# Kernel tuning notes

Measured on AMD Instinct MI355X. Metric: run time of the kernel, lower is better.

Reference implementation:

```python
import jax, jax.numpy as jnp
import numpy as np

B, T, W, L, H, TW = 4, 8192, 1024, 1024, 8, 4
D = L // H
A_SCALE = 8.0  # RG-LRU 'c' constant


def setup_inputs() -> dict:
    key = jax.random.key(0)
    ks = jax.random.split(key, 12)
    nrm = lambda k, shape, std: jax.random.normal(k, shape, jnp.float32) * std
    x = jax.random.normal(ks[0], (B, T, W), jnp.float32)
    segment_pos = jnp.tile(jnp.arange(T, dtype=jnp.int32)[None, :], (B, 1))
    Wy = nrm(ks[1], (W, L), (1.0 / W) ** 0.5)
    by = jnp.zeros((L,), jnp.float32)
    Wx = nrm(ks[2], (W, L), (1.0 / W) ** 0.5)
    bx = jnp.zeros((L,), jnp.float32)
    Wout = nrm(ks[3], (L, W), (1.0 / L) ** 0.5)
    bout = jnp.zeros((W,), jnp.float32)
    conv_w = nrm(ks[4], (TW, L), (1.0 / (TW * L)) ** 0.5)
    conv_b = jnp.zeros((L,), jnp.float32)
    # a_param init: radius in [0.9, 0.999], stored pre-softplus (Griffin rnn_param_init)
    u = jax.random.uniform(ks[5], (L,), jnp.float32)
    a_real = 0.5 * jnp.log(u * (0.999 ** 2 - 0.9 ** 2) + 0.9 ** 2 + 1e-8)  # negative
    a_param = jnp.log(jnp.expm1(-a_real))  # softplus(a_param) == -a_real
    igate_w = nrm(ks[6], (H, D, D), (1.0 / D) ** 0.5)
    igate_b = jnp.zeros((H, D), jnp.float32)
    agate_w = nrm(ks[7], (H, D, D), (1.0 / D) ** 0.5)
    agate_b = jnp.zeros((H, D), jnp.float32)
    return dict(x=x, segment_pos=segment_pos, Wy=Wy, by=by, Wx=Wx, bx=bx,
                conv_w=conv_w, conv_b=conv_b, a_param=a_param,
                igate_w=igate_w, igate_b=igate_b, agate_w=agate_w, agate_b=agate_b,
                Wout=Wout, bout=bout)


def _forward(x, segment_pos, Wy, by, Wx, bx, conv_w, conv_b, a_param,
             igate_w, igate_b, agate_w, agate_b, Wout, bout):
    pos = segment_pos  # [B, T]
    # gating branch
    y = jax.nn.gelu(x @ Wy + by, approximate=True)  # [B,T,L]
    # recurrent branch: linear_x -> causal depthwise conv1d -> RG-LRU
    u = x @ Wx + bx  # [B,T,L]
    acc = jnp.zeros_like(u)
    for i in range(TW):  # small fixed temporal width
        shift = TW - 1 - i
        u_sh = jnp.pad(u, ((0, 0), (shift, 0), (0, 0)))[:, :T]
        valid = (pos >= shift)[..., None]  # zero across segment boundaries
        acc = acc + jnp.where(valid, u_sh * conv_w[i], 0.0)
    u = acc + conv_b  # [B,T,L]
    # RG-LRU gates (block-diagonal per head)
    ur = u.reshape(B, T, H, D)
    gate_x = jax.nn.sigmoid(jnp.einsum('bthd,hde->bthe', ur, igate_w) + igate_b).reshape(B, T, L)
    gate_a = jax.nn.sigmoid(jnp.einsum('bthd,hde->bthe', ur, agate_w) + agate_b).reshape(B, T, L)
    log_a = -A_SCALE * gate_a * jax.nn.softplus(a_param)  # [B,T,L]
    a = jnp.exp(log_a)
    multiplier = jnp.sqrt(1.0 - jnp.exp(2.0 * log_a))
    reset = (pos == 0)[..., None]
    normed_x = (u * gate_x) * jnp.where(reset, 1.0, multiplier)
    a_m = jnp.where(reset, 0.0, a)
    # linear recurrence h_t = a_t * h_{t-1} + normed_x_t via associative scan
    def combine(c1, c2):
        a1, b1 = c1
        a2, b2 = c2
        return (a1 * a2, a2 * b1 + b2)
    _, h = jax.lax.associative_scan(combine, (a_m, normed_x), axis=1)
    return (h * y) @ Wout + bout  # [B,T,W]


def reference(x, segment_pos, Wy, by, Wx, bx, conv_w, conv_b, a_param,
              igate_w, igate_b, agate_w, agate_b, Wout, bout):
    return _forward(x, segment_pos, Wy, by, Wx, bx, conv_w, conv_b, a_param,
                    igate_w, igate_b, agate_w, agate_b, Wout, bout)
```

## Files before the change

kernel.cpp:

```cpp
#include <hip/hip_runtime.h>
#include <cstdint>
#include <cstddef>

#define B_ 4
#define T_ 8192
#define W_ 1024
#define L_ 1024
#define H_ 8
#define D_ 128
#define TW_ 4
#define BT_ (B_*T_)
#define CHUNK_ 32
#define NCH_ (T_/CHUNK_)

typedef __bf16 bf16_t;
typedef __bf16 bf16x8 __attribute__((ext_vector_type(8)));
typedef float  f32x4  __attribute__((ext_vector_type(4)));

__device__ __forceinline__ float  bf2f(bf16_t x){ return (float)x; }
__device__ __forceinline__ bf16_t f2bf(float x){ return (bf16_t)x; }

__device__ __forceinline__ float rcp_ (float x){ return __builtin_amdgcn_rcpf(x); }
__device__ __forceinline__ float sqrt_(float x){ return __builtin_amdgcn_sqrtf(x); }
__device__ __forceinline__ float exp2_(float x){ return __builtin_amdgcn_exp2f(x); }
__device__ __forceinline__ float log2_(float x){ return __builtin_amdgcn_logf(x); }
#define LOG2E_ 1.4426950408889634f

__device__ __forceinline__ float sigmoid_fast(float z){
  return rcp_(1.0f + exp2_(-LOG2E_*z));
}
__device__ __forceinline__ float softplus_fast(float x){
  return (x > 15.0f) ? x : 0.6931471805599453f * log2_(1.0f + exp2_(LOG2E_*x));
}
__device__ __forceinline__ float gelu_fast(float z){
  float g = 0.7978845608028654f*(z + 0.044715f*z*z*z);
  float e = exp2_(-2.8853900817779268f*fabsf(g));
  float th = (1.0f - e)*rcp_(1.0f + e);
  th = copysignf(th, g);
  return 0.5f*z*(1.0f + th);
}

__device__ __forceinline__ void stage16(const bf16_t* g, bf16_t* l){
  __builtin_amdgcn_global_load_lds((const __attribute__((address_space(1))) void*)g,
                                   (__attribute__((address_space(3))) void*)l, 16, 0, 0);
}
__device__ __forceinline__ void stage_tile(const bf16_t* __restrict__ gbase, int ldg,
                                           bf16_t* lds, int wave, int lane){
  #pragma unroll
  for (int c2 = 0; c2 < 2; ++c2){
    int chunk = wave*2 + c2;
    int row = chunk*16 + (lane >> 2);
    int col = (lane & 3)*8;
    stage16(gbase + (size_t)row*ldg + col, lds + chunk*512 + lane*8);
  }
}

__global__ void __launch_bounds__(256) cvt_kernel(const float* __restrict__ in,
                                                  bf16_t* __restrict__ out, int n8){
  int g = blockIdx.x*256 + threadIdx.x;
  if (g >= n8) return;
  f32x4 a = *(const f32x4*)(in + (size_t)g*8);
  f32x4 b = *(const f32x4*)(in + (size_t)g*8 + 4);
  bf16x8 o;
  #pragma unroll
  for (int e=0;e<4;e++){ o[e] = f2bf(a[e]); o[4+e] = f2bf(b[e]); }
  *(bf16x8*)(out + (size_t)g*8) = o;
}

__global__ void __launch_bounds__(256) transpose_f2b(const float* __restrict__ in,
                                                     bf16_t* __restrict__ out, int R, int C){
  __shared__ float tile[32][33];
  size_t mb = (size_t)blockIdx.z * R * C;
  int c0 = blockIdx.x*32, r0 = blockIdx.y*32;
  int tx = threadIdx.x, ty = threadIdx.y;
  #pragma unroll
  for (int i = ty; i < 32; i += 8)
    tile[i][tx] = in[mb + (size_t)(r0+i)*C + c0 + tx];
  __syncthreads();
  #pragma unroll
  for (int i = ty; i < 32; i += 8)
    out[mb + (size_t)(c0+i)*R + r0 + tx] = f2bf(tile[tx][i]);
}

__global__ void __launch_bounds__(256,2) gemm_xw_kernel(
    const bf16_t* __restrict__ X,
    const bf16_t* __restrict__ WyT, const bf16_t* __restrict__ WxT,
    const float* __restrict__ by,  const float* __restrict__ bx,
    bf16_t* __restrict__ Y, bf16_t* __restrict__ U0)
{
  __shared__ __align__(16) bf16_t As [128*32];
  __shared__ __align__(16) bf16_t Bys[128*32];
  __shared__ __align__(16) bf16_t Bxs[128*32];
  __shared__ __align__(16) bf16_t scr_g[4][1280];
  const int K = W_;
  int tid = threadIdx.x, wave = tid>>6, lane = tid&63;
  int wm = wave>>1, wn = wave&1, q = lane>>4, ml = lane&15;
  int lin = blockIdx.x;
  int nl = (lin & 7)*256 + (lin >> 3);
  int bm = nl >> 3, j = nl & 7;
  const bf16_t* Wyp = WyT + (size_t)j*128*K;
  const bf16_t* Wxp = WxT + (size_t)j*128*K;
  f32x4 accY[4][4] = {}, accX[4][4] = {};
  for (int k0 = 0; k0 < K; k0 += 32){
    stage_tile(X + (size_t)bm*128*K + k0, K, As, wave, lane);
    stage_tile(Wyp + k0, K, Bys, wave, lane);
    stage_tile(Wxp + k0, K, Bxs, wave, lane);
    __syncthreads();
    bf16x8 af[4], bvy[4], bvx[4];
    #pragma unroll
    for (int i=0;i<4;i++) af[i]  = *(const bf16x8*)(As  + (wm*64 + i*16 + ml)*32 + q*8);
    #pragma unroll
    for (int i=0;i<4;i++) bvy[i] = *(const bf16x8*)(Bys + (wn*64 + i*16 + ml)*32 + q*8);
    #pragma unroll
    for (int i=0;i<4;i++) bvx[i] = *(const bf16x8*)(Bxs + (wn*64 + i*16 + ml)*32 + q*8);
    #pragma unroll
    for (int i=0;i<4;i++)
      #pragma unroll
      for (int n=0;n<4;n++){
        accY[i][n] = __builtin_amdgcn_mfma_f32_16x16x32_bf16(af[i], bvy[n], accY[i][n], 0,0,0);
        accX[i][n] = __builtin_amdgcn_mfma_f32_16x16x32_bf16(af[i], bvx[n], accX[i][n], 0,0,0);
      }
    __syncthreads();
  }
  float bbY[4], bbX[4];
  #pragma unroll
  for (int n=0;n<4;n++){
    int col = j*128 + wn*64 + n*16 + ml;
    bbY[n] = by[col]; bbX[n] = bx[col];
  }
  bf16_t* s0 = scr_g[wave];
  bf16_t* s1 = s0 + 640;
  int rrow = lane>>2, cgp = lane&3;
  size_t mbase = (size_t)bm*128 + wm*64;
  #pragma unroll
  for (int i=0;i<4;i++){
    size_t grow = mbase + i*16 + rrow;
    int gc = j*128 + wn*64 + cgp*8;
    #pragma unroll
    for (int n=0;n<4;n++){
      bf16_t* sp = (n<2) ? s0 : s1;
      #pragma unroll
      for (int r=0;r<4;r++)
        sp[(q*4+r)*40 + (n&1)*16 + ml] = f2bf(gelu_fast(accY[i][n][r] + bbY[n]));
    }
    {
      bf16x8 v0 = *(const bf16x8*)(s0 + rrow*40 + cgp*8);
      bf16x8 v1 = *(const bf16x8*)(s1 + rrow*40 + cgp*8);
      *(bf16x8*)(Y + grow*L_ + gc)      = v0;
      *(bf16x8*)(Y + grow*L_ + gc + 32) = v1;
    }
    #pragma unroll
    for (int n=0;n<4;n++){
      bf16_t* sp = (n<2) ? s0 : s1;
      #pragma unroll
      for (int r=0;r<4;r++)
        sp[(q*4+r)*40 + (n&1)*16 + ml] = f2bf(accX[i][n][r] + bbX[n]);
    }
    {
      bf16x8 v0 = *(const bf16x8*)(s0 + rrow*40 + cgp*8);
      bf16x8 v1 = *(const bf16x8*)(s1 + rrow*40 + cgp*8);
      *(bf16x8*)(U0 + grow*L_ + gc)      = v0;
      *(bf16x8*)(U0 + grow*L_ + gc + 32) = v1;
    }
  }
}

__global__ void __launch_bounds__(256,2) gate_kernel(
    const bf16_t* __restrict__ U0,
    const bf16_t* __restrict__ igTw, const bf16_t* __restrict__ agTw,
    const float* __restrict__ igb,  const float* __restrict__ agb,
    const float* __restrict__ a_param,
    const float* __restrict__ conv_w, const float* __restrict__ conv_b,
    const int* __restrict__ segpos,
    bf16_t* __restrict__ XN, bf16_t* __restrict__ L2A)
{
  __shared__ __align__(16) bf16_t As[4*128*32];
  __shared__ __align__(16) bf16_t scr_g[4][2560];
  int tid = threadIdx.x, wave = tid>>6, lane = tid&63;
  int wm = wave>>1, wn = wave&1, q = lane>>4, ml = lane&15;
  int bm = blockIdx.x, h = blockIdx.y;

  {
    int cg = tid & 15, rg = tid >> 4;
    int col = cg*8;
    int kcc = col >> 5, c32 = col & 31;
    const bf16_t* up = U0 + ((size_t)bm*128 + (size_t)rg*8)*L_ + h*128 + col;
    f32x4 wta[4], wtb[4];
    #pragma unroll
    for (int s=0;s<4;s++){
      wta[s] = *(const f32x4*)(conv_w + (size_t)(3-s)*L_ + h*128 + col);
      wtb[s] = *(const f32x4*)(conv_w + (size_t)(3-s)*L_ + h*128 + col + 4);
    }
    f32x4 cba = *(const f32x4*)(conv_b + h*128 + col);
    f32x4 cbb = *(const f32x4*)(conv_b + h*128 + col + 4);
    bool first = (bm & 63) == 0;
    int r0 = rg*8;
    bf16x8 zero8 = {};
    bf16x8 m1 = (!first || r0 >= 1) ? *(const bf16x8*)(up - 1*L_) : zero8;
    bf16x8 m2 = (!first || r0 >= 2) ? *(const bf16x8*)(up - 2*L_) : zero8;
    bf16x8 m3 = (!first || r0 >= 3) ? *(const bf16x8*)(up - 3*L_) : zero8;
    #pragma unroll
    for (int r=0;r<8;r++){
      bf16x8 cur = *(const bf16x8*)(up + (size_t)r*L_);
      bf16x8 ov;
      #pragma unroll
      for (int e=0;e<4;e++){
        float v0 = cba[e] + bf2f(cur[e])*wta[0][e] + bf2f(m1[e])*wta[1][e]
                          + bf2f(m2[e])*wta[2][e] + bf2f(m3[e])*wta[3][e];
        float v1 = cbb[e] + bf2f(cur[4+e])*wtb[0][e] + bf2f(m1[4+e])*wtb[1][e]
                          + bf2f(m2[4+e])*wtb[2][e] + bf2f(m3[4+e])*wtb[3][e];
        ov[e] = f2bf(v0); ov[4+e] = f2bf(v1);
      }
      *(bf16x8*)(As + kcc*4096 + (size_t)(r0+r)*32 + c32) = ov;
      m3 = m2; m2 = m1; m1 = cur;
    }
  }
  __syncthreads();

  const bf16_t* igp = igTw + (size_t)h*D_*D_;
  const bf16_t* agp = agTw + (size_t)h*D_*D_;
  f32x4 ax[4][4] = {}, aa[4][4] = {};
  #pragma unroll
  for (int kc=0; kc<4; ++kc){
    bf16x8 af[4], bx_[4], ba_[4];
    #pragma unroll
    for (int i=0;i<4;i++) af[i]  = *(const bf16x8*)(As + kc*4096 + (wm*64 + i*16 + ml)*32 + q*8);
    #pragma unroll
    for (int n=0;n<4;n++) bx_[n] = *(const bf16x8*)(igp + (size_t)(wn*64 + n*16 + ml)*128 + kc*32 + q*8);
    #pragma unroll
    for (int n=0;n<4;n++) ba_[n] = *(const bf16x8*)(agp + (size_t)(wn*64 + n*16 + ml)*128 + kc*32 + q*8);
    #pragma unroll
    for (int i=0;i<4;i++)
      #pragma unroll
      for (int n=0;n<4;n++){
        ax[i][n] = __builtin_amdgcn_mfma_f32_16x16x32_bf16(af[i], bx_[n], ax[i][n], 0,0,0);
        aa[i][n] = __builtin_amdgcn_mfma_f32_16x16x32_bf16(af[i], ba_[n], aa[i][n], 0,0,0);
      }
  }

  bf16_t* sx0 = scr_g[wave];
  bf16_t* sx1 = sx0 + 640;
  bf16_t* sa0 = sx0 + 1280;
  bf16_t* sa1 = sx0 + 1920;
  int rrow = lane>>2, cgp = lane&3;
  size_t mbase = (size_t)bm*128 + wm*64;
  float bb_x[4], bb_a[4], spa4[4]; int kc4[4], ci4[4];
  #pragma unroll
  for (int n=0;n<4;n++){
    int e = wn*64 + n*16 + ml;
    int l = h*D_ + e;
    bb_x[n] = igb[l]; bb_a[n] = agb[l]; spa4[n] = softplus_fast(a_param[l]);
    kc4[n] = e>>5; ci4[n] = e&31;
  }
  #pragma unroll
  for (int i=0;i<4;i++){
    #pragma unroll
    for (int r=0;r<4;r++){
      int rl = wm*64 + i*16 + q*4 + r;
      size_t row = mbase + i*16 + q*4 + r;
      bool reset = (segpos[row] == 0);
      #pragma unroll
      for (int n=0;n<4;n++){
        float uval = bf2f(As[kc4[n]*4096 + rl*32 + ci4[n]]);
        float gx = sigmoid_fast(ax[i][n][r] + bb_x[n]);
        float ga = sigmoid_fast(aa[i][n][r] + bb_a[n]);
        float l2a = -11.541560327111707f * ga * spa4[n];
        float mult = reset ? 1.0f : sqrt_(fmaxf(0.0f, 1.0f - exp2_(2.0f*l2a)));
        bf16_t xnv = f2bf(uval * gx * mult);
        bf16_t lav = f2bf(reset ? -1e30f : l2a);
        int so = (q*4+r)*40 + (n&1)*16 + ml;
        if (n < 2){ sx0[so] = xnv; sa0[so] = lav; }
        else      { sx1[so] = xnv; sa1[so] = lav; }
      }
    }
    size_t grow = mbase + i*16 + rrow;
    int gc = h*D_ + wn*64 + cgp*8;
    bf16x8 xv0 = *(const bf16x8*)(sx0 + rrow*40 + cgp*8);
    bf16x8 xv1 = *(const bf16x8*)(sx1 + rrow*40 + cgp*8);
    *(bf16x8*)(XN + grow*L_ + gc)      = xv0;
    *(bf16x8*)(XN + grow*L_ + gc + 32) = xv1;
    bf16x8 av0 = *(const bf16x8*)(sa0 + rrow*40 + cgp*8);
    bf16x8 av1 = *(const bf16x8*)(sa1 + rrow*40 + cgp*8);
    *(bf16x8*)(L2A + grow*L_ + gc)      = av0;
    *(bf16x8*)(L2A + grow*L_ + gc + 32) = av1;
  }
}

__global__ void __launch_bounds__(128) scan1_kernel(const bf16_t* __restrict__ L2A,
    const bf16_t* __restrict__ XN, float* __restrict__ Aarr, float* __restrict__ Barr)
{
  int lg = threadIdx.x;
  int c = blockIdx.y, b = blockIdx.z;
  int l = lg*8;
  size_t base = ((size_t)b*T_ + (size_t)c*CHUNK_)*L_ + l;
  float suml[8] = {}, brun[8] = {};
  #pragma unroll 4
  for (int t = 0; t < CHUNK_; ++t){
    bf16x8 la = *(const bf16x8*)(L2A + base + (size_t)t*L_);
    bf16x8 xv = *(const bf16x8*)(XN  + base + (size_t)t*L_);
    #pragma unroll
    for (int e=0;e<8;e++){
      float lf = bf2f(la[e]);
      suml[e] += lf;
      brun[e] = exp2_(lf)*brun[e] + bf2f(xv[e]);
    }
  }
  size_t ci = ((size_t)b*NCH_ + c)*L_ + l;
  f32x4 a0, a1, b0, b1;
  #pragma unroll
  for (int e=0;e<4;e++){
    a0[e] = exp2_(suml[e]);   a1[e] = exp2_(suml[4+e]);
    b0[e] = brun[e];          b1[e] = brun[4+e];
  }
  *(f32x4*)(Aarr + ci)     = a0;  *(f32x4*)(Aarr + ci + 4) = a1;
  *(f32x4*)(Barr + ci)     = b0;  *(f32x4*)(Barr + ci + 4) = b1;
}

__global__ void __launch_bounds__(256) scan2_kernel(const float* __restrict__ Aarr,
    const float* __restrict__ Barr, float* __restrict__ Carr)
{
  int l4 = threadIdx.x;
  int b = blockIdx.y;
  f32x4 h = {0.f, 0.f, 0.f, 0.f};
  for (int c = 0; c < NCH_; ++c){
    size_t ci = ((size_t)b*NCH_ + c)*L_ + (size_t)l4*4;
    f32x4 a  = *(const f32x4*)(Aarr + ci);
    f32x4 bb = *(const f32x4*)(Barr + ci);
    *(f32x4*)(Carr + ci) = h;
    #pragma unroll
    for (int e=0;e<4;e++) h[e] = a[e]*h[e] + bb[e];
  }
}

__global__ void __launch_bounds__(128) scan3_kernel(const bf16_t* __restrict__ L2A,
    const bf16_t* __restrict__ XN, const bf16_t* __restrict__ Y,
    const float* __restrict__ Carr, bf16_t* __restrict__ HY)
{
  int lg = threadIdx.x;
  int c = blockIdx.y, b = blockIdx.z;
  int l = lg*8;
  size_t base = ((size_t)b*T_ + (size_t)c*CHUNK_)*L_ + l;
  size_t ci = ((size_t)b*NCH_ + c)*L_ + l;
  f32x4 h0 = *(const f32x4*)(Carr + ci);
  f32x4 h1 = *(const f32x4*)(Carr + ci + 4);
  float h[8];
  #pragma unroll
  for (int e=0;e<4;e++){ h[e] = h0[e]; h[4+e] = h1[e]; }
  #pragma unroll 4
  for (int t = 0; t < CHUNK_; ++t){
    bf16x8 la = *(const bf16x8*)(L2A + base + (size_t)t*L_);
    bf16x8 xv = *(const bf16x8*)(XN  + base + (size_t)t*L_);
    bf16x8 yv = *(const bf16x8*)(Y   + base + (size_t)t*L_);
    bf16x8 o;
    #pragma unroll
    for (int e=0;e<8;e++){
      h[e] = exp2_(bf2f(la[e]))*h[e] + bf2f(xv[e]);
      o[e] = f2bf(h[e]*bf2f(yv[e]));
    }
    *(bf16x8*)(HY + base + (size_t)t*L_) = o;
  }
}

__global__ void __launch_bounds__(256,2) gemm_out_kernel(
    const bf16_t* __restrict__ A_, const bf16_t* __restrict__ WoT,
    const float* __restrict__ bo, float* __restrict__ Out)
{
  __shared__ __align__(16) bf16_t As[128*32];
  __shared__ __align__(16) bf16_t Bs[128*32];
  __shared__ __align__(16) char scr_[4][1280];
  const int K = L_;
  int tid = threadIdx.x, wave = tid>>6, lane = tid&63;
  int wm = wave>>1, wn = wave&1, q = lane>>4, ml = lane&15;
  int lin = blockIdx.x;
  int nl = (lin & 7)*256 + (lin >> 3);
  int bm = nl >> 3, j = nl & 7;
  const bf16_t* Bp = WoT + (size_t)j*128*K;
  f32x4 acc[4][4] = {};
  for (int k0 = 0; k0 < K; k0 += 32){
    stage_tile(A_ + (size_t)bm*128*K + k0, K, As, wave, lane);
    stage_tile(Bp + k0, K, Bs, wave, lane);
    __syncthreads();
    bf16x8 af[4], bv[4];
    #pragma unroll
    for (int i=0;i<4;i++) af[i] = *(const bf16x8*)(As + (wm*64 + i*16 + ml)*32 + q*8);
    #pragma unroll
    for (int i=0;i<4;i++) bv[i] = *(const bf16x8*)(Bs + (wn*64 + i*16 + ml)*32 + q*8);
    #pragma unroll
    for (int i=0;i<4;i++)
      #pragma unroll
      for (int n=0;n<4;n++)
        acc[i][n] = __builtin_amdgcn_mfma_f32_16x16x32_bf16(af[i], bv[n], acc[i][n], 0,0,0);
    __syncthreads();
  }
  float bb[4];
  #pragma unroll
  for (int n=0;n<4;n++) bb[n] = bo[j*128 + wn*64 + n*16 + ml];
  float* scrf = (float*)scr_[wave];
  int rrow = lane>>2, cgp = lane&3;
  size_t mbase = (size_t)bm*128 + wm*64;
  #pragma unroll
  for (int i=0;i<4;i++){
    size_t grow = mbase + i*16 + rrow;
    #pragma unroll
    for (int n=0;n<4;n++){
      #pragma unroll
      for (int r=0;r<4;r++) scrf[(q*4+r)*20 + ml] = acc[i][n][r] + bb[n];
      f32x4 ov = *(const f32x4*)(scrf + rrow*20 + cgp*4);
      *(f32x4*)(Out + grow*W_ + j*128 + wn*64 + n*16 + cgp*4) = ov;
    }
  }
}

extern "C" void kernel_launch(void* const* d_in, const int* in_sizes, int n_in,
                              void* d_out, int out_size, void* d_ws, size_t ws_size,
                              hipStream_t stream)
{
  (void)in_sizes; (void)n_in; (void)out_size;
  const float* x      = (const float*)d_in[0];
  const int*   segpos = (const int*)  d_in[1];
  const float* Wy     = (const float*)d_in[2];
  const float* by     = (const float*)d_in[3];
  const float* Wx     = (const float*)d_in[4];
  const float* bx     = (const float*)d_in[5];
  const float* conv_w = (const float*)d_in[6];
  const float* conv_b = (const float*)d_in[7];
  const float* a_par  = (const float*)d_in[8];
  const float* igw    = (const float*)d_in[9];
  const float* igb    = (const float*)d_in[10];
  const float* agw    = (const float*)d_in[11];
  const float* agb    = (const float*)d_in[12];
  const float* Wout   = (const float*)d_in[13];
  const float* bout   = (const float*)d_in[14];
  float* out = (float*)d_out;

  char* ws = (char*)d_ws;
  size_t off = 0;
  auto alloc = [&](size_t bytes)->void*{ void* p = ws + off; off += (bytes + 255) & ~(size_t)255; return p; };
  bf16_t* Xbf  = (bf16_t*)alloc((size_t)BT_*W_*2);
  bf16_t* WyT  = (bf16_t*)alloc((size_t)W_*L_*2);
  bf16_t* WxT  = (bf16_t*)alloc((size_t)W_*L_*2);
  bf16_t* WoT  = (bf16_t*)alloc((size_t)L_*W_*2);
  bf16_t* igTw = (bf16_t*)alloc((size_t)H_*D_*D_*2);
  bf16_t* agTw = (bf16_t*)alloc((size_t)H_*D_*D_*2);
  bf16_t* Y    = (bf16_t*)alloc((size_t)BT_*L_*2);
  bf16_t* U0   = (bf16_t*)alloc((size_t)BT_*L_*2);
  bf16_t* XN   = (bf16_t*)alloc((size_t)BT_*L_*2);
  float*  Aarr = (float*) alloc((size_t)B_*NCH_*L_*4);
  float*  Barr = (float*) alloc((size_t)B_*NCH_*L_*4);
  float*  Carr = (float*) alloc((size_t)B_*NCH_*L_*4);
  if (ws_size < off) return;

  bf16_t* L2A = Xbf;
  bf16_t* HY  = U0;

  cvt_kernel<<<dim3(BT_*W_/8/256), 256, 0, stream>>>(x, Xbf, BT_*W_/8);

  dim3 tb(32, 8);
  transpose_f2b<<<dim3(32,32,1), tb, 0, stream>>>(Wy,   WyT, 1024, 1024);
  transpose_f2b<<<dim3(32,32,1), tb, 0, stream>>>(Wx,   WxT, 1024, 1024);
  transpose_f2b<<<dim3(32,32,1), tb, 0, stream>>>(Wout, WoT, 1024, 1024);
  transpose_f2b<<<dim3(4,4,H_),  tb, 0, stream>>>(igw,  igTw, 128, 128);
  transpose_f2b<<<dim3(4,4,H_),  tb, 0, stream>>>(agw,  agTw, 128, 128);

  gemm_xw_kernel<<<dim3(2048), 256, 0, stream>>>(Xbf, WyT, WxT, by, bx, Y, U0);
  gate_kernel<<<dim3(BT_/128, H_), 256, 0, stream>>>(U0, igTw, agTw, igb, agb, a_par,
                                                     conv_w, conv_b, segpos, XN, L2A);
  scan1_kernel<<<dim3(1, NCH_, B_), 128, 0, stream>>>(L2A, XN, Aarr, Barr);
  scan2_kernel<<<dim3(1, B_), 256, 0, stream>>>(Aarr, Barr, Carr);
  scan3_kernel<<<dim3(1, NCH_, B_), 128, 0, stream>>>(L2A, XN, Y, Carr, HY);
  gemm_out_kernel<<<dim3(2048), 256, 0, stream>>>(HY, WoT, bout, out);
}
```

Before: 705.0 us.

## Double-buffer GEMM LDS tiles, enlarge scan chunks and spread scan2 across blocks

Both GEMM kernels now use two LDS buffers, loading the next K-slice while MFMAs run on the current one. This drops one barrier per iteration and lets global loads overlap with compute. The chunked scan doubles the chunk length and packs two chunks per 256-thread block. scan2 is split over four 64-thread blocks per batch with an unrolled loop, so the serial pass has more parallelism. The extra LDS doubles shared-memory use per block, which may reduce GEMM occupancy, and the longer chunks lengthen the serial work per thread in scan1 and scan3.

```diff
diff --git a/kernel.cpp b/kernel.cpp
--- a/kernel.cpp
+++ b/kernel.cpp
@@ -10,7 +10,7 @@
 #define D_ 128
 #define TW_ 4
 #define BT_ (B_*T_)
-#define CHUNK_ 32
+#define CHUNK_ 64
 #define NCH_ (T_/CHUNK_)
 
 typedef __bf16 bf16_t;
@@ -88,9 +88,9 @@
     const float* __restrict__ by,  const float* __restrict__ bx,
     bf16_t* __restrict__ Y, bf16_t* __restrict__ U0)
 {
-  __shared__ __align__(16) bf16_t As [128*32];
-  __shared__ __align__(16) bf16_t Bys[128*32];
-  __shared__ __align__(16) bf16_t Bxs[128*32];
+  __shared__ __align__(16) bf16_t As [2][128*32];
+  __shared__ __align__(16) bf16_t Bys[2][128*32];
+  __shared__ __align__(16) bf16_t Bxs[2][128*32];
   __shared__ __align__(16) bf16_t scr_g[4][1280];
   const int K = W_;
   int tid = threadIdx.x, wave = tid>>6, lane = tid&63;
@@ -98,21 +98,29 @@
   int lin = blockIdx.x;
   int nl = (lin & 7)*256 + (lin >> 3);
   int bm = nl >> 3, j = nl & 7;
+  const bf16_t* Xp  = X   + (size_t)bm*128*K;
   const bf16_t* Wyp = WyT + (size_t)j*128*K;
   const bf16_t* Wxp = WxT + (size_t)j*128*K;
   f32x4 accY[4][4] = {}, accX[4][4] = {};
+  stage_tile(Xp,  K, As [0], wave, lane);
+  stage_tile(Wyp, K, Bys[0], wave, lane);
+  stage_tile(Wxp, K, Bxs[0], wave, lane);
+  __syncthreads();
+  int cur = 0;
   for (int k0 = 0; k0 < K; k0 += 32){
-    stage_tile(X + (size_t)bm*128*K + k0, K, As, wave, lane);
-    stage_tile(Wyp + k0, K, Bys, wave, lane);
-    stage_tile(Wxp + k0, K, Bxs, wave, lane);
-    __syncthreads();
+    int nxt = cur ^ 1;
+    if (k0 + 32 < K){
+      stage_tile(Xp  + k0+32, K, As [nxt], wave, lane);
+      stage_tile(Wyp + k0+32, K, Bys[nxt], wave, lane);
+      stage_tile(Wxp + k0+32, K, Bxs[nxt], wave, lane);
+    }
     bf16x8 af[4], bvy[4], bvx[4];
     #pragma unroll
-    for (int i=0;i<4;i++) af[i]  = *(const bf16x8*)(As  + (wm*64 + i*16 + ml)*32 + q*8);
-    #pragma unroll
-    for (int i=0;i<4;i++) bvy[i] = *(const bf16x8*)(Bys + (wn*64 + i*16 + ml)*32 + q*8);
-    #pragma unroll
-    for (int i=0;i<4;i++) bvx[i] = *(const bf16x8*)(Bxs + (wn*64 + i*16 + ml)*32 + q*8);
+    for (int i=0;i<4;i++) af[i]  = *(const bf16x8*)(As [cur] + (wm*64 + i*16 + ml)*32 + q*8);
+    #pragma unroll
+    for (int i=0;i<4;i++) bvy[i] = *(const bf16x8*)(Bys[cur] + (wn*64 + i*16 + ml)*32 + q*8);
+    #pragma unroll
+    for (int i=0;i<4;i++) bvx[i] = *(const bf16x8*)(Bxs[cur] + (wn*64 + i*16 + ml)*32 + q*8);
     #pragma unroll
     for (int i=0;i<4;i++)
       #pragma unroll
@@ -121,6 +129,7 @@
         accX[i][n] = __builtin_amdgcn_mfma_f32_16x16x32_bf16(af[i], bvx[n], accX[i][n], 0,0,0);
       }
     __syncthreads();
+    cur = nxt;
   }
   float bbY[4], bbX[4];
   #pragma unroll
@@ -286,11 +295,12 @@
   }
 }
 
-__global__ void __launch_bounds__(128) scan1_kernel(const bf16_t* __restrict__ L2A,
+__global__ void __launch_bounds__(256) scan1_kernel(const bf16_t* __restrict__ L2A,
     const bf16_t* __restrict__ XN, float* __restrict__ Aarr, float* __restrict__ Barr)
 {
-  int lg = threadIdx.x;
-  int c = blockIdx.y, b = blockIdx.z;
+  int lg = threadIdx.x & 127;
+  int sub = threadIdx.x >> 7;
+  int c = blockIdx.y*2 + sub, b = blockIdx.z;
   int l = lg*8;
   size_t base = ((size_t)b*T_ + (size_t)c*CHUNK_)*L_ + l;
   float suml[8] = {}, brun[8] = {};
@@ -316,12 +326,13 @@
   *(f32x4*)(Barr + ci)     = b0;  *(f32x4*)(Barr + ci + 4) = b1;
 }
 
-__global__ void __launch_bounds__(256) scan2_kernel(const float* __restrict__ Aarr,
+__global__ void __launch_bounds__(64) scan2_kernel(const float* __restrict__ Aarr,
     const float* __restrict__ Barr, float* __restrict__ Carr)
 {
-  int l4 = threadIdx.x;
+  int l4 = blockIdx.x*64 + threadIdx.x;
   int b = blockIdx.y;
   f32x4 h = {0.f, 0.f, 0.f, 0.f};
+  #pragma unroll 4
   for (int c = 0; c < NCH_; ++c){
     size_t ci = ((size_t)b*NCH_ + c)*L_ + (size_t)l4*4;
     f32x4 a  = *(const f32x4*)(Aarr + ci);
@@ -332,12 +343,13 @@
   }
 }
 
-__global__ void __launch_bounds__(128) scan3_kernel(const bf16_t* __restrict__ L2A,
+__global__ void __launch_bounds__(256) scan3_kernel(const bf16_t* __restrict__ L2A,
     const bf16_t* __restrict__ XN, const bf16_t* __restrict__ Y,
     const float* __restrict__ Carr, bf16_t* __restrict__ HY)
 {
-  int lg = threadIdx.x;
-  int c = blockIdx.y, b = blockIdx.z;
+  int lg = threadIdx.x & 127;
+  int sub = threadIdx.x >> 7;
+  int c = blockIdx.y*2 + sub, b = blockIdx.z;
   int l = lg*8;
   size_t base = ((size_t)b*T_ + (size_t)c*CHUNK_)*L_ + l;
   size_t ci = ((size_t)b*NCH_ + c)*L_ + l;
@@ -365,8 +377,8 @@
     const bf16_t* __restrict__ A_, const bf16_t* __restrict__ WoT,
     const float* __restrict__ bo, float* __restrict__ Out)
 {
-  __shared__ __align__(16) bf16_t As[128*32];
-  __shared__ __align__(16) bf16_t Bs[128*32];
+  __shared__ __align__(16) bf16_t As[2][128*32];
+  __shared__ __align__(16) bf16_t Bs[2][128*32];
   __shared__ __align__(16) char scr_[4][1280];
   const int K = L_;
   int tid = threadIdx.x, wave = tid>>6, lane = tid&63;
@@ -374,23 +386,31 @@
   int lin = blockIdx.x;
   int nl = (lin & 7)*256 + (lin >> 3);
   int bm = nl >> 3, j = nl & 7;
+  const bf16_t* Ap = A_  + (size_t)bm*128*K;
   const bf16_t* Bp = WoT + (size_t)j*128*K;
   f32x4 acc[4][4] = {};
+  stage_tile(Ap, K, As[0], wave, lane);
+  stage_tile(Bp, K, Bs[0], wave, lane);
+  __syncthreads();
+  int cur = 0;
   for (int k0 = 0; k0 < K; k0 += 32){
-    stage_tile(A_ + (size_t)bm*128*K + k0, K, As, wave, lane);
-    stage_tile(Bp + k0, K, Bs, wave, lane);
-    __syncthreads();
+    int nxt = cur ^ 1;
+    if (k0 + 32 < K){
+      stage_tile(Ap + k0+32, K, As[nxt], wave, lane);
+      stage_tile(Bp + k0+32, K, Bs[nxt], wave, lane);
+    }
     bf16x8 af[4], bv[4];
     #pragma unroll
-    for (int i=0;i<4;i++) af[i] = *(const bf16x8*)(As + (wm*64 + i*16 + ml)*32 + q*8);
-    #pragma unroll
-    for (int i=0;i<4;i++) bv[i] = *(const bf16x8*)(Bs + (wn*64 + i*16 + ml)*32 + q*8);
+    for (int i=0;i<4;i++) af[i] = *(const bf16x8*)(As[cur] + (wm*64 + i*16 + ml)*32 + q*8);
+    #pragma unroll
+    for (int i=0;i<4;i++) bv[i] = *(const bf16x8*)(Bs[cur] + (wn*64 + i*16 + ml)*32 + q*8);
     #pragma unroll
     for (int i=0;i<4;i++)
       #pragma unroll
       for (int n=0;n<4;n++)
         acc[i][n] = __builtin_amdgcn_mfma_f32_16x16x32_bf16(af[i], bv[n], acc[i][n], 0,0,0);
     __syncthreads();
+    cur = nxt;
   }
   float bb[4];
   #pragma unroll
@@ -465,8 +485,8 @@
   gemm_xw_kernel<<<dim3(2048), 256, 0, stream>>>(Xbf, WyT, WxT, by, bx, Y, U0);
   gate_kernel<<<dim3(BT_/128, H_), 256, 0, stream>>>(U0, igTw, agTw, igb, agb, a_par,
                                                      conv_w, conv_b, segpos, XN, L2A);
-  scan1_kernel<<<dim3(1, NCH_, B_), 128, 0, stream>>>(L2A, XN, Aarr, Barr);
-  scan2_kernel<<<dim3(1, B_), 256, 0, stream>>>(Aarr, Barr, Carr);
-  scan3_kernel<<<dim3(1, NCH_, B_), 128, 0, stream>>>(L2A, XN, Y, Carr, HY);
+  scan1_kernel<<<dim3(1, NCH_/2, B_), 256, 0, stream>>>(L2A, XN, Aarr, Barr);
+  scan2_kernel<<<dim3(4, B_), 64, 0, stream>>>(Aarr, Barr, Carr);
+  scan3_kernel<<<dim3(1, NCH_/2, B_), 256, 0, stream>>>(L2A, XN, Y, Carr, HY);
   gemm_out_kernel<<<dim3(2048), 256, 0, stream>>>(HY, WoT, bout, out);
 }
```

Result: no change. 702.3 us (-0.4%).
